# Performance work log

Hardware: AMD Instinct MI355X
Metric: run time of the kernel (lower is better)

Reference implementation:

```python
import jax, jax.numpy as jnp
import numpy as np

N, IN_DIM, HID, Z, HEADS, E = 10000, 128, 128, 64, 4, 320000
NEG_SLOPE = 0.2


def setup_inputs() -> dict:
    key = jax.random.key(0)
    ks = jax.random.split(key, 16)
    s = 0.1
    return {
        "x": jax.random.normal(ks[0], (N, IN_DIM), jnp.float32),
        "edge_index": jax.random.randint(ks[1], (2, E), 0, N, jnp.int64),
        "gcn_w": jax.random.normal(ks[2], (IN_DIM, HID), jnp.float32) * s,
        "gcn_b": jnp.zeros((HID,), jnp.float32),
        "gat_w": jax.random.normal(ks[3], (HID, HEADS * HID), jnp.float32) * s,
        "gat_att_src": jax.random.normal(ks[4], (HEADS, HID), jnp.float32) * s,
        "gat_att_dst": jax.random.normal(ks[5], (HEADS, HID), jnp.float32) * s,
        "gat_b": jnp.zeros((HID,), jnp.float32),
        "mlp_w1": jax.random.normal(ks[6], (HID, HID), jnp.float32) * s,
        "mlp_b1": jnp.zeros((HID,), jnp.float32),
        "mlp_w2": jax.random.normal(ks[7], (HID, HID), jnp.float32) * s,
        "mlp_b2": jnp.zeros((HID,), jnp.float32),
        "mu_w": jax.random.normal(ks[8], (HID, Z), jnp.float32) * s,
        "mu_b": jnp.zeros((Z,), jnp.float32),
        "lv_w": jax.random.normal(ks[9], (HID, Z), jnp.float32) * s,
        "lv_b": jnp.zeros((Z,), jnp.float32),
    }


def _add_self_loops(edge_index, n):
    loop = jnp.arange(n, dtype=edge_index.dtype)
    src = jnp.concatenate([edge_index[0], loop])
    dst = jnp.concatenate([edge_index[1], loop])
    return src, dst


def _gcn(x, edge_index, w, b):
    # PyG GCNConv: add self-loops, symmetric normalization D^-1/2 (A+I) D^-1/2
    n = x.shape[0]
    src, dst = _add_self_loops(edge_index, n)
    deg = jax.ops.segment_sum(jnp.ones_like(dst, dtype=x.dtype), dst, num_segments=n)
    dinv = jax.lax.rsqrt(deg)  # deg >= 1 due to self-loops
    norm = dinv[src] * dinv[dst]  # [E+N]
    h = x @ w  # [N, HID]
    out = jax.ops.segment_sum(h[src] * norm[:, None], dst, num_segments=n)
    return out + b


def _gat(x, edge_index, w, att_src, att_dst, b):
    # PyG GATConv(heads=HEADS, concat=False): average heads, self-loops added
    n = x.shape[0]
    src, dst = _add_self_loops(edge_index, n)
    h = (x @ w).reshape(n, HEADS, HID)  # [N, H, C]
    a_src = jnp.einsum('nhc,hc->nh', h, att_src)  # [N, H]
    a_dst = jnp.einsum('nhc,hc->nh', h, att_dst)
    e = jax.nn.leaky_relu(a_src[src] + a_dst[dst], NEG_SLOPE)  # [E+N, H]
    # segment softmax over incoming edges of each destination node
    emax = jax.ops.segment_max(e, dst, num_segments=n)
    e = jnp.exp(e - emax[dst])
    denom = jax.ops.segment_sum(e, dst, num_segments=n)
    alpha = e / denom[dst]  # [E+N, H]
    out = jax.ops.segment_sum(h[src] * alpha[:, :, None], dst, num_segments=n)  # [N, H, C]
    return out.mean(axis=1) + b


def reference(x, edge_index, gcn_w, gcn_b, gat_w, gat_att_src, gat_att_dst, gat_b,
              mlp_w1, mlp_b1, mlp_w2, mlp_b2, mu_w, mu_b, lv_w, lv_b):
    h = jax.nn.relu(_gcn(x, edge_index, gcn_w, gcn_b))
    h = jax.nn.relu(_gat(h, edge_index, gat_w, gat_att_src, gat_att_dst, gat_b))
    h = jax.nn.relu(h @ mlp_w1 + mlp_b1)
    h = jax.nn.relu(h @ mlp_w2 + mlp_b2)
    mu = h @ mu_w + mu_b
    logvar = h @ lv_w + lv_b
    return (mu, logvar)
```

## Files before the change

### kernel.cpp

```cpp
#include <hip/hip_runtime.h>

#define NN 10000
#define D 128
#define NH 4
#define HD 512
#define ZD 64

__device__ __forceinline__ float lrelu(float x){ return x > 0.0f ? x : 0.2f*x; }

__global__ __launch_bounds__(256) void k_hist(const int* __restrict__ dst,
                                              int* __restrict__ deg, int E){
  int i = blockIdx.x*256 + threadIdx.x;
  if (i < E) atomicAdd(&deg[dst[i]], 1);
}

__global__ __launch_bounds__(1024) void k_scan(int* __restrict__ deg,
                                               int* __restrict__ ioff,
                                               float* __restrict__ dinv){
  __shared__ int part[1024];
  const int tid = threadIdx.x;
  const int base = tid*10;
  int local[10]; int s = 0;
#pragma unroll
  for (int i=0;i<10;i++){
    int idx = base+i;
    int v = (idx < NN) ? deg[idx] : 0;
    if (idx < NN) dinv[idx] = rsqrtf(1.0f + (float)v);
    local[i] = s; s += v;
  }
  part[tid] = s;
  __syncthreads();
  for (int o=1;o<1024;o<<=1){
    int v = (tid>=o) ? part[tid-o] : 0;
    __syncthreads();
    part[tid] += v;
    __syncthreads();
  }
  int excl = part[tid] - s;
#pragma unroll
  for (int i=0;i<10;i++){
    int idx = base+i;
    if (idx < NN){
      int o = excl + local[i];
      ioff[idx] = o;
      deg[idx]  = o;
    }
  }
  if (tid == 1023) ioff[NN] = part[1023];
}

__global__ __launch_bounds__(256) void k_fill(const int* __restrict__ src,
                                              const int* __restrict__ dst,
                                              int* __restrict__ cur,
                                              int* __restrict__ csr, int E,
                                              float* __restrict__ az){
  int i = blockIdx.x*256 + threadIdx.x;
  if (i < NN*NH*2) az[i] = 0.f;
  if (i >= E) return;
  int pos = atomicAdd(&cur[dst[i]], 1);
  csr[pos] = src[i];
}

__global__ __launch_bounds__(256) void k_mega(const float* __restrict__ x,
                                              const float* __restrict__ gcn_w,
                                              float* __restrict__ xw,
                                              const float* __restrict__ gat_w,
                                              const float* __restrict__ att_src,
                                              const float* __restrict__ att_dst,
                                              float* __restrict__ w_as,
                                              float* __restrict__ w_ad,
                                              int* __restrict__ icur){
  __shared__ float As[64][132];
  __shared__ float Ws[128][68];
  const int bx  = blockIdx.x;
  const int tid = threadIdx.x;
  if (bx < 314){
    const int row0 = (bx >> 1)*64;
    const int col0 = (bx & 1)*64;
#pragma unroll
    for (int i=0;i<8;i++){
      int f  = tid + i*256;
      int r  = f >> 5;
      int k4 = (f & 31) << 2;
      int rr = row0 + r;
      float4 v = make_float4(0.f,0.f,0.f,0.f);
      if (rr < NN) v = *(const float4*)&x[rr*D + k4];
      *(float4*)&As[r][k4] = v;
    }
#pragma unroll
    for (int i=0;i<8;i++){
      int f  = tid + i*256;
      int k  = f >> 4;
      int c4 = (f & 15) << 2;
      *(float4*)&Ws[k][c4] = *(const float4*)&gcn_w[k*D + col0 + c4];
    }
    __syncthreads();
    const int tx = tid & 15, ty = tid >> 4;
    float acc[4][4] = {{0.f}};
#pragma unroll 4
    for (int k=0;k<128;k++){
      float4 w = *(const float4*)&Ws[k][tx<<2];
      float wv[4] = {w.x, w.y, w.z, w.w};
      float av[4];
#pragma unroll
      for (int i=0;i<4;i++) av[i] = As[(ty<<2)+i][k];
#pragma unroll
      for (int i=0;i<4;i++)
#pragma unroll
        for (int j=0;j<4;j++) acc[i][j] = fmaf(av[i], wv[j], acc[i][j]);
    }
#pragma unroll
    for (int i=0;i<4;i++){
      int r = row0 + (ty<<2) + i;
      if (r >= NN) continue;
#pragma unroll
      for (int j=0;j<4;j++)
        xw[r*D + col0 + (tx<<2) + j] = acc[i][j];
    }
  } else if (bx < 318){
    const int h = bx - 314;
    const int k = tid;
    if (k < 128){
      const float* wrow = &gat_w[k*HD + h*D];
      const float* as   = &att_src[h*D];
      const float* ad   = &att_dst[h*D];
      float s = 0.f, d = 0.f;
#pragma unroll 4
      for (int c=0;c<D;c++){
        float wv = wrow[c];
        s = fmaf(wv, as[c], s);
        d = fmaf(wv, ad[c], d);
      }
      w_as[h*D + k] = s;
      w_ad[h*D + k] = d;
    }
  } else {
    int i = (bx - 318)*256 + tid;
    if (i < NN) icur[i] = 0;
  }
}

__global__ __launch_bounds__(256) void k_gcn_agg(const float* __restrict__ xw,
                                                 const float* __restrict__ dinv,
                                                 const int* __restrict__ ioff,
                                                 const int* __restrict__ csr,
                                                 const float* __restrict__ bias,
                                                 const float* __restrict__ w_as,
                                                 const float* __restrict__ w_ad,
                                                 float* __restrict__ out,
                                                 float* __restrict__ a_src,
                                                 float* __restrict__ a_dst){
  __shared__ float2 snm[4][64];
  const int sub  = blockIdx.x & 7;
  const int ch   = sub >> 2;
  const int g    = blockIdx.x >> 3;
  const int wv   = threadIdx.x >> 6;
  const int lane = threadIdx.x & 63;
  const int w    = g*16 + (sub & 3)*4 + wv;
  const int c    = ch*64 + lane;
  const int beg = ioff[w], end = ioff[w+1];
  float din = dinv[w];
  float ax = xw[w*D + c] * din;
  for (int jb = beg; jb < end; jb += 64){
    int cnt = end - jb; if (cnt > 64) cnt = 64;
    if (lane < cnt){
      int s = csr[jb + lane];
      snm[wv][lane] = make_float2(dinv[s], __int_as_float(s));
    }
    __builtin_amdgcn_wave_barrier();
#pragma unroll 4
    for (int l=0; l<cnt; l++){
      float2 t = snm[wv][l];
      int ss = __float_as_int(t.y);
      ax = fmaf(t.x, xw[ss*D + c], ax);
    }
    __builtin_amdgcn_wave_barrier();
  }
  float val = fmaxf(fmaf(ax, din, bias[c]), 0.f);
  out[w*D + c] = val;
  float ps[NH], pd[NH];
#pragma unroll
  for (int h=0;h<NH;h++){
    ps[h] = val * w_as[h*D + c];
    pd[h] = val * w_ad[h*D + c];
  }
#pragma unroll
  for (int o=32;o>0;o>>=1){
#pragma unroll
    for (int h=0;h<NH;h++){
      ps[h] += __shfl_xor(ps[h], o);
      pd[h] += __shfl_xor(pd[h], o);
    }
  }
  if (lane == 0){
#pragma unroll
    for (int h=0;h<NH;h++){
      atomicAdd(&a_src[w*4 + h], ps[h]);
      atomicAdd(&a_dst[w*4 + h], pd[h]);
    }
  }
}

__global__ __launch_bounds__(256) void k_gat_agg2(const float* __restrict__ h1,
                                                  const float* __restrict__ a_src,
                                                  const float* __restrict__ a_dst,
                                                  const int* __restrict__ ioff,
                                                  const int* __restrict__ csr,
                                                  float* __restrict__ agg){
  __shared__ float4 sal[4][64];
  __shared__ int    ssr[4][64];
  const int sub  = blockIdx.x & 7;
  const int ch   = sub >> 2;
  const int g    = blockIdx.x >> 3;
  const int wv   = threadIdx.x >> 6;
  const int lane = threadIdx.x & 63;
  const int w    = g*16 + (sub & 3)*4 + wv;
  const int c    = ch*64 + lane;
  const int beg = ioff[w], end = ioff[w+1];
  float4 ad  = *(const float4*)&a_dst[w*4];
  float4 asn = *(const float4*)&a_src[w*4];
  float e0 = __expf(lrelu(asn.x + ad.x));
  float e1 = __expf(lrelu(asn.y + ad.y));
  float e2 = __expf(lrelu(asn.z + ad.z));
  float e3 = __expf(lrelu(asn.w + ad.w));
  float hv = h1[w*D + c];
  float o0 = e0*hv, o1 = e1*hv, o2 = e2*hv, o3 = e3*hv;
  float den0=0.f, den1=0.f, den2=0.f, den3=0.f;

  for (int jb = beg; jb < end; jb += 64){
    int cnt = end - jb; if (cnt > 64) cnt = 64;
    if (lane < cnt){
      int s = csr[jb + lane];
      float4 as = *(const float4*)&a_src[s*4];
      float g0 = __expf(lrelu(as.x + ad.x));
      float g1 = __expf(lrelu(as.y + ad.y));
      float g2 = __expf(lrelu(as.z + ad.z));
      float g3 = __expf(lrelu(as.w + ad.w));
      sal[wv][lane] = make_float4(g0,g1,g2,g3);
      ssr[wv][lane] = s;
      den0 += g0; den1 += g1; den2 += g2; den3 += g3;
    }
    __builtin_amdgcn_wave_barrier();
#pragma unroll 4
    for (int l=0; l<cnt; l++){
      float4 b = sal[wv][l];
      float sv = h1[ssr[wv][l]*D + c];
      o0 = fmaf(b.x, sv, o0);
      o1 = fmaf(b.y, sv, o1);
      o2 = fmaf(b.z, sv, o2);
      o3 = fmaf(b.w, sv, o3);
    }
    __builtin_amdgcn_wave_barrier();
  }
#pragma unroll
  for (int o=32; o>0; o>>=1){
    den0 += __shfl_xor(den0, o);
    den1 += __shfl_xor(den1, o);
    den2 += __shfl_xor(den2, o);
    den3 += __shfl_xor(den3, o);
  }
  den0 += e0; den1 += e1; den2 += e2; den3 += e3;
  float* ab = &agg[(size_t)w*HD + c];
  ab[0*D] = o0 * (0.25f/den0);
  ab[1*D] = o1 * (0.25f/den1);
  ab[2*D] = o2 * (0.25f/den2);
  ab[3*D] = o3 * (0.25f/den3);
}

#define KLOOP4(WB, LDW)                                                     \
  _Pragma("unroll 2")                                                       \
  for (int k4=0; k4<128; k4+=4){                                            \
    float4 w0 = *(const float4*)&(WB)[(k4+0)*(LDW)];                        \
    float4 w1 = *(const float4*)&(WB)[(k4+1)*(LDW)];                        \
    float4 w2 = *(const float4*)&(WB)[(k4+2)*(LDW)];                        \
    float4 w3 = *(const float4*)&(WB)[(k4+3)*(LDW)];                        \
    _Pragma("unroll")                                                       \
    for (int i=0;i<4;i++){                                                  \
      float4 sv = *(const float4*)&S[r0+i][k4];                             \
      acc[i][0]=fmaf(sv.w,w3.x,fmaf(sv.z,w2.x,fmaf(sv.y,w1.x,fmaf(sv.x,w0.x,acc[i][0])))); \
      acc[i][1]=fmaf(sv.w,w3.y,fmaf(sv.z,w2.y,fmaf(sv.y,w1.y,fmaf(sv.x,w0.y,acc[i][1])))); \
      acc[i][2]=fmaf(sv.w,w3.z,fmaf(sv.z,w2.z,fmaf(sv.y,w1.z,fmaf(sv.x,w0.z,acc[i][2])))); \
      acc[i][3]=fmaf(sv.w,w3.w,fmaf(sv.z,w2.w,fmaf(sv.y,w1.w,fmaf(sv.x,w0.w,acc[i][3])))); \
    }                                                                       \
  }

__global__ __launch_bounds__(128) void k_gat_mlp(const float* __restrict__ agg,
                                                 const float* __restrict__ gat_w,
                                                 const float* __restrict__ gat_b,
                                                 const float* __restrict__ w1,
                                                 const float* __restrict__ b1,
                                                 const float* __restrict__ w2,
                                                 const float* __restrict__ b2,
                                                 const float* __restrict__ wmu,
                                                 const float* __restrict__ bmu,
                                                 const float* __restrict__ wlv,
                                                 const float* __restrict__ blv,
                                                 float* __restrict__ out){
  __shared__ float S[16][132];
  const int tid  = threadIdx.x;
  const int tx   = tid & 31;
  const int ty   = tid >> 5;
  const int c0   = tx << 2;
  const int r0   = ty << 2;
  const int row0 = blockIdx.x*16;
  float acc[4][4] = {{0.f}};

  for (int h=0; h<NH; h++){
    __syncthreads();
#pragma unroll
    for (int i=0;i<4;i++){
      int f  = tid + i*128;
      int r  = f >> 5;
      int k4 = (f & 31) << 2;
      *(float4*)&S[r][k4] = *(const float4*)&agg[(size_t)(row0+r)*HD + h*D + k4];
    }
    __syncthreads();
    const float* Wb = &gat_w[h*D + c0];
    KLOOP4(Wb, HD)
  }
  __syncthreads();
#pragma unroll
  for (int i=0;i<4;i++)
#pragma unroll
    for (int j=0;j<4;j++){
      S[r0+i][c0+j] = fmaxf(acc[i][j] + gat_b[c0+j], 0.f);
      acc[i][j] = 0.f;
    }

  for (int layer=0; layer<2; layer++){
    const float* W  = layer ? w2 : w1;
    const float* bb = layer ? b2 : b1;
    __syncthreads();
    const float* Wb = &W[c0];
    KLOOP4(Wb, D)
    __syncthreads();
#pragma unroll
    for (int i=0;i<4;i++)
#pragma unroll
      for (int j=0;j<4;j++){
        S[r0+i][c0+j] = fmaxf(acc[i][j] + bb[c0+j], 0.f);
        acc[i][j] = 0.f;
      }
  }

  __syncthreads();
  {
    const int hd = tx >> 4;
    const int cl = (tx & 15) << 2;
    const float* Wb = (hd ? &wlv[cl] : &wmu[cl]);
    const float* bb = hd ? blv : bmu;
    float* ob = out + (size_t)hd*NN*ZD;
    KLOOP4(Wb, ZD)
#pragma unroll
    for (int i=0;i<4;i++){
      int r = row0 + r0 + i;
      float4 v = make_float4(acc[i][0] + bb[cl+0],
                             acc[i][1] + bb[cl+1],
                             acc[i][2] + bb[cl+2],
                             acc[i][3] + bb[cl+3]);
      *(float4*)&ob[r*ZD + cl] = v;
    }
  }
}

extern "C" void kernel_launch(void* const* d_in, const int* in_sizes, int n_in,
                              void* d_out, int out_size, void* d_ws, size_t ws_size,
                              hipStream_t stream){
  const float* x     = (const float*)d_in[0];
  const int*   ei    = (const int*)d_in[1];
  const float* gcn_w = (const float*)d_in[2];
  const float* gcn_b = (const float*)d_in[3];
  const float* gat_w = (const float*)d_in[4];
  const float* att_s = (const float*)d_in[5];
  const float* att_d = (const float*)d_in[6];
  const float* gat_b = (const float*)d_in[7];
  const float* w1    = (const float*)d_in[8];
  const float* b1    = (const float*)d_in[9];
  const float* w2    = (const float*)d_in[10];
  const float* b2    = (const float*)d_in[11];
  const float* mu_w  = (const float*)d_in[12];
  const float* mu_b  = (const float*)d_in[13];
  const float* lv_w  = (const float*)d_in[14];
  const float* lv_b  = (const float*)d_in[15];
  const int E = in_sizes[1] / 2;
  const int* src = ei;
  const int* dst = ei + E;

  float* ws    = (float*)d_ws;
  float* xw    = ws;
  float* h1    = xw + NN*D;
  float* agg   = h1 + NN*D;
  float* dinv  = agg + (size_t)NN*HD;
  float* w_as  = dinv + NN;
  float* w_ad  = w_as + HD;
  float* a_src = w_ad + HD;
  float* a_dst = a_src + NN*NH;
  int*   ioff  = (int*)(a_dst + NN*NH);
  int*   icur  = ioff + NN + 1;
  int*   csr   = icur + NN;

  const int gE = (E + 255)/256;

  k_mega<<<358, 256, 0, stream>>>(x, gcn_w, xw, gat_w, att_s, att_d,
                                  w_as, w_ad, icur);
  k_hist<<<gE, 256, 0, stream>>>(dst, icur, E);
  k_scan<<<1, 1024, 0, stream>>>(icur, ioff, dinv);
  k_fill<<<gE, 256, 0, stream>>>(src, dst, icur, csr, E, a_src);

  k_gcn_agg<<<(NN/16)*8, 256, 0, stream>>>(xw, dinv, ioff, csr, gcn_b,
                                           w_as, w_ad, h1, a_src, a_dst);
  k_gat_agg2<<<(NN/16)*8, 256, 0, stream>>>(h1, a_src, a_dst, ioff, csr, agg);
  k_gat_mlp<<<NN/16, 128, 0, stream>>>(agg, gat_w, gat_b, w1, b1, w2, b2,
                                       mu_w, mu_b, lv_w, lv_b, (float*)d_out);
}
```

Baseline: 179.5 us.

## Fuse degree histogram into mega kernel and widen MLP blocks with prefetched weights

The separate histogram kernel is removed. Its atomic degree counting now runs in extra blocks of the mega GEMM kernel, and the counter zeroing becomes a memset. This saves one launch and lets the histogram overlap with the GEMM blocks. The final MLP kernel moves to 256 threads with 2 rows per thread, which halves register accumulators and raises occupancy. Its inner weight loop now software-prefetches the next weight float4s, at the cost of extra registers and an added memset call.

```diff
diff --git a/kernel.cpp b/kernel.cpp
--- a/kernel.cpp
+++ b/kernel.cpp
@@ -7,12 +7,6 @@
 #define ZD 64
 
 __device__ __forceinline__ float lrelu(float x){ return x > 0.0f ? x : 0.2f*x; }
-
-__global__ __launch_bounds__(256) void k_hist(const int* __restrict__ dst,
-                                              int* __restrict__ deg, int E){
-  int i = blockIdx.x*256 + threadIdx.x;
-  if (i < E) atomicAdd(&deg[dst[i]], 1);
-}
 
 __global__ __launch_bounds__(1024) void k_scan(int* __restrict__ deg,
                                                int* __restrict__ ioff,
@@ -69,7 +63,8 @@
                                               const float* __restrict__ att_dst,
                                               float* __restrict__ w_as,
                                               float* __restrict__ w_ad,
-                                              int* __restrict__ icur){
+                                              const int* __restrict__ dst,
+                                              int* __restrict__ icur, int E){
   __shared__ float As[64][132];
   __shared__ float Ws[128][68];
   const int bx  = blockIdx.x;
@@ -136,7 +131,7 @@
     }
   } else {
     int i = (bx - 318)*256 + tid;
-    if (i < NN) icur[i] = 0;
+    if (i < E) atomicAdd(&icur[dst[i]], 1);
   }
 }
 
@@ -268,23 +263,31 @@
 }
 
 #define KLOOP4(WB, LDW)                                                     \
-  _Pragma("unroll 2")                                                       \
-  for (int k4=0; k4<128; k4+=4){                                            \
-    float4 w0 = *(const float4*)&(WB)[(k4+0)*(LDW)];                        \
-    float4 w1 = *(const float4*)&(WB)[(k4+1)*(LDW)];                        \
-    float4 w2 = *(const float4*)&(WB)[(k4+2)*(LDW)];                        \
-    float4 w3 = *(const float4*)&(WB)[(k4+3)*(LDW)];                        \
-    _Pragma("unroll")                                                       \
-    for (int i=0;i<4;i++){                                                  \
-      float4 sv = *(const float4*)&S[r0+i][k4];                             \
-      acc[i][0]=fmaf(sv.w,w3.x,fmaf(sv.z,w2.x,fmaf(sv.y,w1.x,fmaf(sv.x,w0.x,acc[i][0])))); \
-      acc[i][1]=fmaf(sv.w,w3.y,fmaf(sv.z,w2.y,fmaf(sv.y,w1.y,fmaf(sv.x,w0.y,acc[i][1])))); \
-      acc[i][2]=fmaf(sv.w,w3.z,fmaf(sv.z,w2.z,fmaf(sv.y,w1.z,fmaf(sv.x,w0.z,acc[i][2])))); \
-      acc[i][3]=fmaf(sv.w,w3.w,fmaf(sv.z,w2.w,fmaf(sv.y,w1.w,fmaf(sv.x,w0.w,acc[i][3])))); \
+  {                                                                         \
+    float4 cw0 = *(const float4*)&(WB)[0*(LDW)];                            \
+    float4 cw1 = *(const float4*)&(WB)[1*(LDW)];                            \
+    float4 cw2 = *(const float4*)&(WB)[2*(LDW)];                            \
+    float4 cw3 = *(const float4*)&(WB)[3*(LDW)];                            \
+    _Pragma("unroll 4")                                                     \
+    for (int k4=0; k4<128; k4+=4){                                          \
+      int kp = (k4+4 < 128) ? (k4+4) : 124;                                 \
+      float4 nw0 = *(const float4*)&(WB)[(kp+0)*(LDW)];                     \
+      float4 nw1 = *(const float4*)&(WB)[(kp+1)*(LDW)];                     \
+      float4 nw2 = *(const float4*)&(WB)[(kp+2)*(LDW)];                     \
+      float4 nw3 = *(const float4*)&(WB)[(kp+3)*(LDW)];                     \
+      _Pragma("unroll")                                                     \
+      for (int i=0;i<2;i++){                                                \
+        float4 sv = *(const float4*)&S[r0+i][k4];                           \
+        acc[i][0]=fmaf(sv.w,cw3.x,fmaf(sv.z,cw2.x,fmaf(sv.y,cw1.x,fmaf(sv.x,cw0.x,acc[i][0])))); \
+        acc[i][1]=fmaf(sv.w,cw3.y,fmaf(sv.z,cw2.y,fmaf(sv.y,cw1.y,fmaf(sv.x,cw0.y,acc[i][1])))); \
+        acc[i][2]=fmaf(sv.w,cw3.z,fmaf(sv.z,cw2.z,fmaf(sv.y,cw1.z,fmaf(sv.x,cw0.z,acc[i][2])))); \
+        acc[i][3]=fmaf(sv.w,cw3.w,fmaf(sv.z,cw2.w,fmaf(sv.y,cw1.w,fmaf(sv.x,cw0.w,acc[i][3])))); \
+      }                                                                     \
+      cw0=nw0; cw1=nw1; cw2=nw2; cw3=nw3;                                   \
     }                                                                       \
   }
 
-__global__ __launch_bounds__(128) void k_gat_mlp(const float* __restrict__ agg,
+__global__ __launch_bounds__(256) void k_gat_mlp(const float* __restrict__ agg,
                                                  const float* __restrict__ gat_w,
                                                  const float* __restrict__ gat_b,
                                                  const float* __restrict__ w1,
@@ -301,15 +304,15 @@
   const int tx   = tid & 31;
   const int ty   = tid >> 5;
   const int c0   = tx << 2;
-  const int r0   = ty << 2;
+  const int r0   = ty << 1;
   const int row0 = blockIdx.x*16;
-  float acc[4][4] = {{0.f}};
+  float acc[2][4] = {{0.f}};
 
   for (int h=0; h<NH; h++){
     __syncthreads();
 #pragma unroll
-    for (int i=0;i<4;i++){
-      int f  = tid + i*128;
+    for (int i=0;i<2;i++){
+      int f  = tid + i*256;
       int r  = f >> 5;
       int k4 = (f & 31) << 2;
       *(float4*)&S[r][k4] = *(const float4*)&agg[(size_t)(row0+r)*HD + h*D + k4];
@@ -320,7 +323,7 @@
   }
   __syncthreads();
 #pragma unroll
-  for (int i=0;i<4;i++)
+  for (int i=0;i<2;i++)
 #pragma unroll
     for (int j=0;j<4;j++){
       S[r0+i][c0+j] = fmaxf(acc[i][j] + gat_b[c0+j], 0.f);
@@ -335,7 +338,7 @@
     KLOOP4(Wb, D)
     __syncthreads();
 #pragma unroll
-    for (int i=0;i<4;i++)
+    for (int i=0;i<2;i++)
 #pragma unroll
       for (int j=0;j<4;j++){
         S[r0+i][c0+j] = fmaxf(acc[i][j] + bb[c0+j], 0.f);
@@ -352,7 +355,7 @@
     float* ob = out + (size_t)hd*NN*ZD;
     KLOOP4(Wb, ZD)
 #pragma unroll
-    for (int i=0;i<4;i++){
+    for (int i=0;i<2;i++){
       int r = row0 + r0 + i;
       float4 v = make_float4(acc[i][0] + bb[cl+0],
                              acc[i][1] + bb[cl+1],
@@ -401,15 +404,16 @@
 
   const int gE = (E + 255)/256;
 
-  k_mega<<<358, 256, 0, stream>>>(x, gcn_w, xw, gat_w, att_s, att_d,
-                                  w_as, w_ad, icur);
-  k_hist<<<gE, 256, 0, stream>>>(dst, icur, E);
+  hipMemsetAsync(icur, 0, NN*sizeof(int), stream);
+
+  k_mega<<<318 + gE, 256, 0, stream>>>(x, gcn_w, xw, gat_w, att_s, att_d,
+                                       w_as, w_ad, dst, icur, E);
   k_scan<<<1, 1024, 0, stream>>>(icur, ioff, dinv);
   k_fill<<<gE, 256, 0, stream>>>(src, dst, icur, csr, E, a_src);
 
   k_gcn_agg<<<(NN/16)*8, 256, 0, stream>>>(xw, dinv, ioff, csr, gcn_b,
                                            w_as, w_ad, h1, a_src, a_dst);
   k_gat_agg2<<<(NN/16)*8, 256, 0, stream>>>(h1, a_src, a_dst, ioff, csr, agg);
-  k_gat_mlp<<<NN/16, 128, 0, stream>>>(agg, gat_w, gat_b, w1, b1, w2, b2,
+  k_gat_mlp<<<NN/16, 256, 0, stream>>>(agg, gat_w, gat_b, w1, b1, w2, b2,
                                        mu_w, mu_b, lv_w, lv_b, (float*)d_out);
 }
```

New measurement: 196.1 us. 1.09x slower.
